# Kernel optimization log

Measured on AMD Instinct MI355X. Metric: run time of the kernel, lower is better.

## Reference

```python
import jax, jax.numpy as jnp
import numpy as np

N = 4
KERNEL_SIZE = 3
DISP_RANK = 2
D_IN = 128
BATCH = 262144
PERTURBATION_SCALE = 0.1


def _group_constants():
    # Kernel neighborhood: identity, swap(0,1), sign-flip of element 0
    identity = np.eye(N, dtype=np.float32)
    swap01 = np.eye(N, dtype=np.float32)[[1, 0, 2, 3]]
    signflip0 = np.eye(N, dtype=np.float32)
    signflip0[0, 0] = -1.0
    kernel = np.stack([identity, swap01, signflip0])  # (3,4,4)
    # Anchor elements: 3-cycle (0->1->2->0, 3 fixed) and 4-cycle (0->1->2->3->0)
    c3 = np.zeros((N, N), dtype=np.float32)
    c3[0, 1] = 1.0; c3[1, 2] = 1.0; c3[2, 0] = 1.0; c3[3, 3] = 1.0
    c4 = np.zeros((N, N), dtype=np.float32)
    c4[0, 1] = 1.0; c4[1, 2] = 1.0; c4[2, 3] = 1.0; c4[3, 0] = 1.0
    anchors = np.stack([c3, c4])  # (2,4,4)
    return jnp.asarray(kernel), jnp.asarray(anchors)

KERNEL_MATS, ANCHOR_MATS = _group_constants()


def setup_inputs() -> dict:
    key = jax.random.key(0)
    ks = jax.random.split(key, 8)
    scale = 1.0 / np.sqrt(D_IN)
    return {
        "h": jax.random.normal(ks[0], (BATCH, N), dtype=jnp.float32),
        "x": jax.random.normal(ks[1], (BATCH, D_IN), dtype=jnp.float32),
        "W_alpha": jax.random.normal(ks[2], (KERNEL_SIZE, D_IN), dtype=jnp.float32) * scale,
        "b_alpha": jnp.zeros((KERNEL_SIZE,), dtype=jnp.float32),
        "W_a": jax.random.normal(ks[3], (DISP_RANK * N, D_IN), dtype=jnp.float32) * scale,
        "b_a": jnp.zeros((DISP_RANK * N,), dtype=jnp.float32),
        "W_B": jax.random.normal(ks[4], (N, D_IN), dtype=jnp.float32) * scale,
        "b_B": jnp.zeros((N,), dtype=jnp.float32),
    }


def reference(h, x, W_alpha, b_alpha, W_a, b_a, W_B, b_B):
    batch = h.shape[0]
    # alpha: softmax over kernel neighborhood weights, (batch, k)
    alpha = jax.nn.softmax(x @ W_alpha.T + b_alpha, axis=-1)
    # Weighted sum of kernel group matrices: (batch, n, n)
    A = jnp.einsum('bk,kij->bij', alpha, KERNEL_MATS)
    # Low-rank tanh perturbation: a: (batch, r, n); row-scaled anchor matrices
    a = jnp.tanh(x @ W_a.T + b_a).reshape(batch, DISP_RANK, N) * PERTURBATION_SCALE
    A = A + jnp.einsum('bri,rij->bij', a, ANCHOR_MATS)
    # h_new = A h + B x
    h_new = jnp.einsum('bij,bj->bi', A, h) + x @ W_B.T + b_B
    return h_new
```

## Files before the change

### kernel.cpp

```cpp
#include <hip/hip_runtime.h>


using f32x4  = __attribute__((ext_vector_type(4))) float;
using bf16x8 = __attribute__((ext_vector_type(8))) short;

__device__ __forceinline__ short f2bf(float f) {
    union { float f; unsigned u; } v; v.f = f;
    unsigned u = v.u + 0x7fffu + ((v.u >> 16) & 1u);
    return (short)(u >> 16);
}

__device__ __forceinline__ bf16x8 pack8(float4 a, float4 b) {
    bf16x8 r;
    r[0] = f2bf(a.x); r[1] = f2bf(a.y); r[2] = f2bf(a.z); r[3] = f2bf(a.w);
    r[4] = f2bf(b.x); r[5] = f2bf(b.y); r[6] = f2bf(b.z); r[7] = f2bf(b.w);
    return r;
}

constexpr int TPB = 64;

__global__ __launch_bounds__(TPB) void gmdr_mfma_kernel(
    const float* __restrict__ h,
    const float* __restrict__ x,
    const float* __restrict__ W_alpha, const float* __restrict__ b_alpha,
    const float* __restrict__ W_a,     const float* __restrict__ b_a,
    const float* __restrict__ W_B,     const float* __restrict__ b_B,
    float* __restrict__ out, int batch)
{
    __shared__ float pt[4 * 328];

    const int lane = threadIdx.x;
    const int n16  = lane & 15;
    const int g    = lane >> 4;
    const long base = (long)blockIdx.x * 64;

    bf16x8 wb[4];
#pragma unroll
    for (int s = 0; s < 4; ++s) wb[s] = (bf16x8){};
    {
        const float* wrow = nullptr;
        if (n16 < 3)       wrow = W_alpha + n16 * 128;
        else if (n16 < 11) wrow = W_a + (n16 - 3) * 128;
        else if (n16 < 15) wrow = W_B + (n16 - 11) * 128;
        if (wrow) {
            const float4* wp = reinterpret_cast<const float4*>(wrow);
#pragma unroll
            for (int s = 0; s < 4; ++s)
                wb[s] = pack8(wp[2 * g + 8 * s], wp[2 * g + 8 * s + 1]);
        }
    }

    const float4* __restrict__ X4 = reinterpret_cast<const float4*>(x);

    f32x4 acc[4];
#pragma unroll
    for (int t = 0; t < 4; ++t) {
        acc[t] = (f32x4){};
        long rowA = base + t * 16 + n16;
        if (rowA >= batch) rowA = batch - 1;
        const float4* xp = X4 + rowA * 32 + 2 * g;
#pragma unroll
        for (int s = 0; s < 4; ++s) {
            const bf16x8 af = pack8(xp[8 * s], xp[8 * s + 1]);
            acc[t] = __builtin_amdgcn_mfma_f32_16x16x32_bf16(af, wb[s], acc[t], 0, 0, 0);
        }
    }

#pragma unroll
    for (int t = 0; t < 4; ++t)
#pragma unroll
        for (int r = 0; r < 4; ++r)
            pt[t * 328 + (g * 4 + r) * 20 + n16] = acc[t][r];
    __syncthreads();

    const long row = base + lane;
    if (row < batch) {
        const float4* pr = reinterpret_cast<const float4*>(
            &pt[(lane >> 4) * 328 + (lane & 15) * 20]);
        const float4 pa = pr[0], pb = pr[1], pc = pr[2], pd = pr[3];

        const float l0 = pa.x + b_alpha[0];
        const float l1 = pa.y + b_alpha[1];
        const float l2 = pa.z + b_alpha[2];
        const float m  = fmaxf(l0, fmaxf(l1, l2));
        const float e0 = __expf(l0 - m);
        const float e1 = __expf(l1 - m);
        const float e2 = __expf(l2 - m);
        const float inv = 1.0f / (e0 + e1 + e2);
        const float al0 = e0 * inv, al1 = e1 * inv, al2 = e2 * inv;

        const float pv[8] = { pa.w, pb.x, pb.y, pb.z, pb.w, pc.x, pc.y, pc.z };
        float tq[8];
#pragma unroll
        for (int i = 0; i < 8; ++i) {
            const float v = pv[i] + b_a[i];
            tq[i] = (1.0f - 2.0f / (__expf(2.0f * v) + 1.0f)) * 0.1f;
        }

        const float4 hv = reinterpret_cast<const float4*>(h)[row];

        const float asum = al0 + al1 + al2;
        const float r0 = (al0 - al2) * hv.x + al1 * hv.y + (tq[0] + tq[4]) * hv.y;
        const float r1 = al1 * hv.x + (al0 + al2) * hv.y + (tq[1] + tq[5]) * hv.z;
        const float r2 = asum * hv.z + tq[2] * hv.x + tq[6] * hv.w;
        const float r3 = asum * hv.w + tq[3] * hv.w + tq[7] * hv.x;

        float4 ov;
        ov.x = r0 + pc.w + b_B[0];
        ov.y = r1 + pd.x + b_B[1];
        ov.z = r2 + pd.y + b_B[2];
        ov.w = r3 + pd.z + b_B[3];
        reinterpret_cast<float4*>(out)[row] = ov;
    }
}

extern "C" void kernel_launch(void* const* d_in, const int* in_sizes, int n_in,
                              void* d_out, int out_size, void* d_ws, size_t ws_size,
                              hipStream_t stream) {
    const float* h       = (const float*)d_in[0];
    const float* x       = (const float*)d_in[1];
    const float* W_alpha = (const float*)d_in[2];
    const float* b_alpha = (const float*)d_in[3];
    const float* W_a     = (const float*)d_in[4];
    const float* b_a     = (const float*)d_in[5];
    const float* W_B     = (const float*)d_in[6];
    const float* b_B     = (const float*)d_in[7];
    float* out = (float*)d_out;

    const int batch = in_sizes[0] / 4;
    const int grid  = (batch + TPB - 1) / TPB;

    gmdr_mfma_kernel<<<grid, TPB, 0, stream>>>(
        h, x, W_alpha, b_alpha, W_a, b_a, W_B, b_B, out, batch);
}
```

Baseline: 207.7 us.

## Use 4-wave blocks, double-buffer x tile loads, and prefetch h early

Blocks grow from one wavefront to four, each wave handling its own 64 rows, so each workgroup covers 256 rows and the grid shrinks fourfold. The x loads for the next 16-row tile are issued into a second register buffer before the current tile's MFMAs run. The h load moves ahead of the LDS store and barrier so its latency overlaps. Register use rises from holding two 8-float4 buffers, and the barrier now spans four waves.

Result: no change. 208.5 us (+0.4%).

```diff
diff --git a/kernel.cpp b/kernel.cpp
--- a/kernel.cpp
+++ b/kernel.cpp
@@ -17,7 +17,7 @@
     return r;
 }
 
-constexpr int TPB = 64;
+constexpr int TPB = 256;
 
 __global__ __launch_bounds__(TPB) void gmdr_mfma_kernel(
     const float* __restrict__ h,
@@ -27,12 +27,14 @@
     const float* __restrict__ W_B,     const float* __restrict__ b_B,
     float* __restrict__ out, int batch)
 {
-    __shared__ float pt[4 * 328];
+    __shared__ float pt[16 * 328];
 
-    const int lane = threadIdx.x;
+    const int tid  = threadIdx.x;
+    const int lane = tid & 63;
+    const int wid  = tid >> 6;
     const int n16  = lane & 15;
     const int g    = lane >> 4;
-    const long base = (long)blockIdx.x * 64;
+    const long wbase = (long)blockIdx.x * 256 + wid * 64;
 
     bf16x8 wb[4];
 #pragma unroll
@@ -52,31 +54,48 @@
 
     const float4* __restrict__ X4 = reinterpret_cast<const float4*>(x);
 
+    auto rowptr = [&](int t) {
+        long rowA = wbase + t * 16 + n16;
+        if (rowA >= batch) rowA = batch - 1;
+        return X4 + rowA * 32 + 2 * g;
+    };
+
     f32x4 acc[4];
 #pragma unroll
-    for (int t = 0; t < 4; ++t) {
-        acc[t] = (f32x4){};
-        long rowA = base + t * 16 + n16;
-        if (rowA >= batch) rowA = batch - 1;
-        const float4* xp = X4 + rowA * 32 + 2 * g;
-#pragma unroll
-        for (int s = 0; s < 4; ++s) {
-            const bf16x8 af = pack8(xp[8 * s], xp[8 * s + 1]);
-            acc[t] = __builtin_amdgcn_mfma_f32_16x16x32_bf16(af, wb[s], acc[t], 0, 0, 0);
-        }
-    }
+    for (int t = 0; t < 4; ++t) acc[t] = (f32x4){};
+
+    float4 bufA[8], bufB[8];
+
+#define LOADT(buf, t) { const float4* xp = rowptr(t);                          \
+    _Pragma("unroll") for (int s = 0; s < 4; ++s) {                            \
+        buf[2*s] = xp[8*s]; buf[2*s+1] = xp[8*s+1]; } }
+
+#define COMPT(buf, t) { _Pragma("unroll") for (int s = 0; s < 4; ++s) {        \
+        const bf16x8 af = pack8(buf[2*s], buf[2*s+1]);                         \
+        acc[t] = __builtin_amdgcn_mfma_f32_16x16x32_bf16(af, wb[s], acc[t], 0, 0, 0); } }
+
+    LOADT(bufA, 0)
+    LOADT(bufB, 1)  COMPT(bufA, 0)
+    LOADT(bufA, 2)  COMPT(bufB, 1)
+    LOADT(bufB, 3)  COMPT(bufA, 2)
+                    COMPT(bufB, 3)
+#undef LOADT
+#undef COMPT
+
+    const long row = wbase + lane;
+    float4 hv = make_float4(0.f, 0.f, 0.f, 0.f);
+    if (row < batch) hv = reinterpret_cast<const float4*>(h)[row];
 
 #pragma unroll
     for (int t = 0; t < 4; ++t)
 #pragma unroll
         for (int r = 0; r < 4; ++r)
-            pt[t * 328 + (g * 4 + r) * 20 + n16] = acc[t][r];
+            pt[(wid * 4 + t) * 328 + (g * 4 + r) * 20 + n16] = acc[t][r];
     __syncthreads();
 
-    const long row = base + lane;
     if (row < batch) {
         const float4* pr = reinterpret_cast<const float4*>(
-            &pt[(lane >> 4) * 328 + (lane & 15) * 20]);
+            &pt[(wid * 4 + (lane >> 4)) * 328 + (lane & 15) * 20]);
         const float4 pa = pr[0], pb = pr[1], pc = pr[2], pd = pr[3];
 
         const float l0 = pa.x + b_alpha[0];
@@ -96,8 +115,6 @@
             const float v = pv[i] + b_a[i];
             tq[i] = (1.0f - 2.0f / (__expf(2.0f * v) + 1.0f)) * 0.1f;
         }
-
-        const float4 hv = reinterpret_cast<const float4*>(h)[row];
 
         const float asum = al0 + al1 + al2;
         const float r0 = (al0 - al2) * hv.x + al1 * hv.y + (tq[0] + tq[4]) * hv.y;
@@ -128,7 +145,7 @@
     float* out = (float*)d_out;
 
     const int batch = in_sizes[0] / 4;
-    const int grid  = (batch + TPB - 1) / TPB;
+    const int grid  = (batch + 255) / 256;
 
     gmdr_mfma_kernel<<<grid, TPB, 0, stream>>>(
         h, x, W_alpha, b_alpha, W_a, b_a, W_B, b_B, out, batch);
```
